# Optimization experiments

Hardware: AMD Instinct MI355X
Metric: run time of the kernel (lower is better)

Reference implementation:

```python
import jax, jax.numpy as jnp
import numpy as np

B, T, F, U = 64, 256, 64, 512  # batch, bid_sequence, features, lstm units


def setup_inputs() -> dict:
    key = jax.random.key(0)
    ks = jax.random.split(key, 8)
    sc = 0.05
    return {
        "inputs": jax.random.normal(ks[0], (B, T, F), jnp.float32),
        "kernel": jax.random.normal(ks[1], (F, 4 * U), jnp.float32) * sc,      # LSTM input kernel (i,f,c,o)
        "rec_kernel": jax.random.normal(ks[2], (U, 4 * U), jnp.float32) * sc,  # LSTM recurrent kernel
        "bias": jax.random.normal(ks[3], (4 * U,), jnp.float32) * sc,          # LSTM bias
        "att_W": jax.random.normal(ks[4], (T, T), jnp.float32) * sc,           # row t = weights of attention_denses[t] (first t cols used)
        "att_b": jax.random.normal(ks[5], (T,), jnp.float32) * sc,             # bias of attention_denses[t]
        "out_W": jax.random.normal(ks[6], (U,), jnp.float32) * sc,             # final Dense(1) kernel
        "out_b": jax.random.normal(ks[7], (), jnp.float32) * sc,               # final Dense(1) bias
    }


def reference(inputs, kernel, rec_kernel, bias, att_W, att_b, out_W, out_b):
    Bs, Ts, _ = inputs.shape
    Us = rec_kernel.shape[0]

    # ---- LSTM (keras LSTMCell, gate order i,f,c,o; sigmoid/tanh) ----
    xz = jnp.einsum('btf,fg->btg', inputs, kernel) + bias  # precompute input projection

    def step(carry, z):
        h, c = carry
        g = z + h @ rec_kernel
        i, f, gc, o = jnp.split(g, 4, axis=-1)
        c = jax.nn.sigmoid(f) * c + jax.nn.sigmoid(i) * jnp.tanh(gc)
        h = jax.nn.sigmoid(o) * jnp.tanh(c)
        return (h, c), h

    init = (jnp.zeros((Bs, Us), inputs.dtype), jnp.zeros((Bs, Us), inputs.dtype))
    _, hs = jax.lax.scan(step, init, jnp.swapaxes(xz, 0, 1))
    x = jnp.swapaxes(hs, 0, 1)  # (B, T, U)

    # ---- attention_loop ----
    # keras Attention([x[:t], [x[t]]]) softmaxes over a single key -> weights are
    # exactly 1, so attn output is x[t] tiled t times; transpose + Dense_t(1)
    # collapses to sum(att_W[t, :t]) * x[t] + att_b[t]. Step 0 passes x[0] through.
    t_idx = jnp.arange(Ts)
    tri = (t_idx[None, :] < t_idx[:, None]).astype(x.dtype)  # row t: first t cols valid
    coef = jnp.where(t_idx == 0, jnp.asarray(1.0, x.dtype), jnp.sum(att_W * tri, axis=1))
    shift = jnp.where(t_idx == 0, jnp.asarray(0.0, x.dtype), att_b)
    att = x * coef[None, :, None] + shift[None, :, None]  # (B, T, U)

    # ---- final Dense(1) + reshape + sigmoid ----
    return jax.nn.sigmoid(jnp.einsum('btu,u->bt', att, out_W) + out_b)  # (B, T)
```

## Files before the change

kernel.cpp:

```cpp
#include <hip/hip_runtime.h>
#include <hip/hip_bf16.h>
#include <string.h>

#define B_ 64
#define T_ 256
#define F_ 64
#define U_ 512
#define G4_ 2048
#define KTOT 576
#define KSTEPS 18

typedef __attribute__((ext_vector_type(8))) short short8;
typedef __attribute__((ext_vector_type(4))) float v4f;
typedef __attribute__((ext_vector_type(4))) int i4;
typedef unsigned short u16;

__device__ __forceinline__ float bf2f(u16 b) {
    unsigned int x = ((unsigned int)b) << 16;
    float f; memcpy(&f, &x, 4); return f;
}
__device__ __forceinline__ u16 f2bf(float f) {
    __hip_bfloat16 h = __float2bfloat16(f);
    u16 b; memcpy(&b, &h, 2); return b;
}
__device__ __forceinline__ float sigmoidf_(float x) { return 1.f / (1.f + __expf(-x)); }
__device__ __forceinline__ float tanhf_(float x) {
    float xc = fminf(15.f, fmaxf(-15.f, x));
    float e = __expf(2.f * xc);
    return (e - 1.f) / (e + 1.f);
}

__device__ __forceinline__ float ldany(const void* p, size_t i, int fg) {
    return fg ? ((const float*)p)[i] : bf2f(((const u16*)p)[i]);
}

#define WS_FLAG   0
#define WS_XB     64
#define WS_WP     2097216
#define WS_H2     4456512
#define WS_DOT    4718656
#define WS_BIASF  4784192
#define WS_ATTWF  4792384
#define WS_ATTBF  5054528
#define WS_OUTWF  5055552
#define WS_OUTBF  5057600
#define WS_NEED   5057920

__global__ __launch_bounds__(256) void detect(const unsigned int* __restrict__ w,
                                              int* __restrict__ flag) {
    __shared__ int votes;
    if (threadIdx.x == 0) votes = 0;
    __syncthreads();
    unsigned int v = w[threadIdx.x];
    int e = (v >> 7) & 0xFF;
    if (e >= 100 && e <= 135) atomicAdd(&votes, 1);
    __syncthreads();
    if (threadIdx.x == 0) *flag = (votes < 200) ? 1 : 0;
}

__global__ __launch_bounds__(256) void convert(const void* __restrict__ x,
                                               const void* __restrict__ bias,
                                               const void* __restrict__ attW,
                                               const void* __restrict__ attb,
                                               const void* __restrict__ outW,
                                               const void* __restrict__ outb,
                                               const int* __restrict__ flag,
                                               u16* __restrict__ xb,
                                               float* __restrict__ biasf,
                                               float* __restrict__ attWf,
                                               float* __restrict__ attbf,
                                               float* __restrict__ outWf,
                                               float* __restrict__ outbf,
                                               float* __restrict__ dot,
                                               unsigned int* __restrict__ h2z) {
    int fg = *flag;
    size_t i = (size_t)blockIdx.x * 256 + threadIdx.x;
    if (i < 1048576) {
        float v = ldany(x, i, fg);
        int b = (int)(i >> 14), t = (int)((i >> 6) & 255), f = (int)(i & 63);
        xb[((size_t)t * B_ + b) * F_ + f] = f2bf(v);
        return;
    }
    i -= 1048576;
    if (i < 2048)  { biasf[i] = ldany(bias, i, fg); return; }
    i -= 2048;
    if (i < 65536) { attWf[i] = ldany(attW, i, fg); return; }
    i -= 65536;
    if (i < 256)   { attbf[i] = ldany(attb, i, fg); return; }
    i -= 256;
    if (i < 512)   { outWf[i] = ldany(outW, i, fg); return; }
    i -= 512;
    if (i < 1)     { outbf[i] = ldany(outb, i, fg); return; }
    i -= 1;
    if (i < 16384) { dot[i] = 0.f; return; }
    i -= 16384;
    if (i < 32768) { h2z[i] = 0u; return; }
}

__global__ __launch_bounds__(256) void pack_w(const void* __restrict__ kin,
                                              const void* __restrict__ krec,
                                              const int* __restrict__ flag,
                                              u16* __restrict__ Wp) {
    int fg = *flag;
    int gid = blockIdx.x * 256 + threadIdx.x;
    int lane = gid & 63;
    int frag = gid >> 6;
    int nt = frag / KSTEPS;
    int ks = frag - nt * KSTEPS;
    int kbase = ks * 32 + (lane >> 4) * 8;
    int cp = nt * 16 + (lane & 15);
    int u = cp >> 2, gate = cp & 3;
    int C = gate * U_ + u;
    short8 v;
    for (int j = 0; j < 8; j++) {
        int k = kbase + j;
        float w = (k < F_) ? ldany(kin, (size_t)k * G4_ + C, fg)
                           : ldany(krec, (size_t)(k - F_) * G4_ + C, fg);
        v[j] = (short)f2bf(w);
    }
    *reinterpret_cast<short8*>(Wp + (size_t)gid * 8) = v;
}

__global__ __launch_bounds__(512, 2) void lstm_persist(const u16* __restrict__ xb,
                                                       const float* __restrict__ biasf,
                                                       const float* __restrict__ outWf,
                                                       const u16* __restrict__ Wp,
                                                       u16* __restrict__ h2,
                                                       float* __restrict__ dot) {
    __shared__ __align__(16) u16 stage[16 * 520];
    __shared__ __align__(16) float gbuf[16][164];
    __shared__ float dp[32][16];

    int tid = threadIdx.x;
    int bid = blockIdx.x;
    int rg = bid & 3;
    int gu = bid >> 2;
    int w = tid >> 6, l = tid & 63;
    int nt = gu * 8 + w;

    short8 W[KSTEPS];
    #pragma unroll
    for (int ks = 0; ks < KSTEPS; ks++)
        W[ks] = *reinterpret_cast<const short8*>(Wp + ((size_t)(nt * KSTEPS + ks) * 64 + l) * 8);

    int arow = rg * 16 + (l & 15);
    int koff = (l >> 4) * 8;
    int plr = 2 * w + (l >> 5);
    int pcol = (l & 31) * 16;
    int er = tid >> 5;
    int ui = tid & 31;
    int unit = gu * 32 + ui;
    float bia = biasf[0 * U_ + unit], bif = biasf[1 * U_ + unit];
    float big = biasf[2 * U_ + unit], bio = biasf[3 * U_ + unit];
    float wout = outWf[unit];
    float c = 0.f;

    for (int t = 0; t < T_; t++) {
        u16* hcur = h2 + (size_t)(t & 1) * (B_ * U_);
        const u16* hprev = h2 + (size_t)((t + 1) & 1) * (B_ * U_);
        unsigned int wtag = ((unsigned)(t >> 1) & 1u) ^ 1u;
        unsigned int rpat = ((((unsigned)(t - 1) >> 1) & 1u) ^ 1u) * 0x00010001u;

        i4 q0, q1;
        {
            const void* bp = (const void*)(hprev + (size_t)(rg * 16 + plr) * U_ + pcol);
            int spins = 0;
            for (;;) {
                asm volatile(
                    "global_load_dwordx4 %0, %2, off sc0 sc1\n\t"
                    "global_load_dwordx4 %1, %2, off offset:16 sc0 sc1\n\t"
                    "s_waitcnt vmcnt(0)"
                    : "=v"(q0), "=v"(q1) : "v"(bp) : "memory");
                if (t == 0) break;
                unsigned bad = 0;
                bad |= (((unsigned)q0[0]) ^ rpat) & 0x00010001u;
                bad |= (((unsigned)q0[1]) ^ rpat) & 0x00010001u;
                bad |= (((unsigned)q0[2]) ^ rpat) & 0x00010001u;
                bad |= (((unsigned)q0[3]) ^ rpat) & 0x00010001u;
                bad |= (((unsigned)q1[0]) ^ rpat) & 0x00010001u;
                bad |= (((unsigned)q1[1]) ^ rpat) & 0x00010001u;
                bad |= (((unsigned)q1[2]) ^ rpat) & 0x00010001u;
                bad |= (((unsigned)q1[3]) ^ rpat) & 0x00010001u;
                if (__ballot(bad == 0) == ~0ull) break;
                if (++spins > (1 << 14)) break;
                __builtin_amdgcn_s_sleep(2);
            }
        }
        *reinterpret_cast<i4*>(&stage[plr * 520 + pcol])     = q0;
        *reinterpret_cast<i4*>(&stage[plr * 520 + pcol + 8]) = q1;
        __syncthreads();

        const u16* xrow = xb + ((size_t)t * B_ + arow) * F_;
        short8 a0 = *reinterpret_cast<const short8*>(xrow + koff);
        short8 a1 = *reinterpret_cast<const short8*>(xrow + 32 + koff);
        v4f acc0 = {0.f, 0.f, 0.f, 0.f}, acc1 = {0.f, 0.f, 0.f, 0.f};
        acc0 = __builtin_amdgcn_mfma_f32_16x16x32_bf16(a0, W[0], acc0, 0, 0, 0);
        acc1 = __builtin_amdgcn_mfma_f32_16x16x32_bf16(a1, W[1], acc1, 0, 0, 0);
        #pragma unroll
        for (int ks = 2; ks < KSTEPS; ks += 2) {
            short8 ah0 = *reinterpret_cast<const short8*>(
                &stage[(l & 15) * 520 + (ks - 2) * 32 + koff]);
            short8 ah1 = *reinterpret_cast<const short8*>(
                &stage[(l & 15) * 520 + (ks - 1) * 32 + koff]);
            acc0 = __builtin_amdgcn_mfma_f32_16x16x32_bf16(ah0, W[ks],     acc0, 0, 0, 0);
            acc1 = __builtin_amdgcn_mfma_f32_16x16x32_bf16(ah1, W[ks + 1], acc1, 0, 0, 0);
        }
        v4f acc = acc0 + acc1;

        {
            int c0 = 16 * w + (l & 15);
            int coff = 5 * (c0 >> 2) + (c0 & 3);
            int rb = (l >> 4) * 4;
            #pragma unroll
            for (int rr = 0; rr < 4; rr++)
                gbuf[rb + rr][coff] = acc[rr];
        }
        __syncthreads();

        {
            const float* gr = &gbuf[er][5 * ui];
            float ig = sigmoidf_(gr[0] + bia);
            float fg = sigmoidf_(gr[1] + bif);
            float gc = tanhf_(gr[2] + big);
            float og = sigmoidf_(gr[3] + bio);
            c = fg * c + ig * gc;
            float h = og * tanhf_(c);

            float hp = __shfl_xor(h, 1, 64);
            if ((ui & 1) == 0) {
                unsigned int pk = (unsigned int)(((unsigned)f2bf(h)  & 0xFFFEu) | wtag)
                                | ((unsigned int)(((unsigned)f2bf(hp) & 0xFFFEu) | wtag) << 16);
                void* sp = (void*)(hcur + (size_t)(rg * 16 + er) * U_ + unit);
                asm volatile("global_store_dword %0, %1, off sc0 sc1"
                             :: "v"(sp), "v"(pk) : "memory");
            }

            float s = h * wout;
            s += __shfl_xor(s, 1, 64);
            s += __shfl_xor(s, 2, 64);
            s += __shfl_xor(s, 4, 64);
            s += __shfl_xor(s, 8, 64);
            s += __shfl_xor(s, 16, 64);
            if (ui == 0) dp[t & 31][er] = s;
        }

        if ((t & 31) == 31) {
            __syncthreads();
            int t0 = t - 31;
            int tt = tid >> 4, row = tid & 15;
            atomicAdd(&dot[(size_t)(rg * 16 + row) * T_ + (t0 + tt)], dp[tt][row]);
        }
    }
}

__global__ __launch_bounds__(256) void finale(const float* __restrict__ attWf,
                                              const float* __restrict__ attbf,
                                              const float* __restrict__ outWf,
                                              const float* __restrict__ outbf,
                                              const float* __restrict__ dot,
                                              const int* __restrict__ flag,
                                              void* __restrict__ out) {
    __shared__ float red[256];
    int t = blockIdx.x, tid = threadIdx.x;
    int fg = *flag;

    float v = (tid < t) ? attWf[(size_t)t * T_ + tid] : 0.f;
    red[tid] = v; __syncthreads();
    for (int s = 128; s > 0; s >>= 1) { if (tid < s) red[tid] += red[tid + s]; __syncthreads(); }
    float coef = (t == 0) ? 1.f : red[0];
    __syncthreads();
    red[tid] = outWf[tid] + outWf[tid + 256]; __syncthreads();
    for (int s = 128; s > 0; s >>= 1) { if (tid < s) red[tid] += red[tid + s]; __syncthreads(); }
    float sumW = red[0];

    float base = ((t == 0) ? 0.f : attbf[t]) * sumW + outbf[0];

    if (tid < B_) {
        float s = sigmoidf_(coef * dot[(size_t)tid * T_ + t] + base);
        size_t idx = (size_t)tid * T_ + t;
        if (fg) ((float*)out)[idx] = s;
        else    ((u16*)out)[idx] = f2bf(s);
    }
}

extern "C" void kernel_launch(void* const* d_in, const int* in_sizes, int n_in,
                              void* d_out, int out_size, void* d_ws, size_t ws_size,
                              hipStream_t stream) {
    const void* x    = d_in[0];
    const void* kin  = d_in[1];
    const void* krec = d_in[2];
    const void* bias = d_in[3];
    const void* attW = d_in[4];
    const void* attb = d_in[5];
    const void* outW = d_in[6];
    const void* outb = d_in[7];

    if (ws_size < (size_t)WS_NEED) return;

    char* ws = (char*)d_ws;
    int*   flag  = (int*)(ws + WS_FLAG);
    u16*   xb    = (u16*)(ws + WS_XB);
    u16*   Wp    = (u16*)(ws + WS_WP);
    u16*   h2    = (u16*)(ws + WS_H2);
    float* dot   = (float*)(ws + WS_DOT);
    float* biasf = (float*)(ws + WS_BIASF);
    float* attWf = (float*)(ws + WS_ATTWF);
    float* attbf = (float*)(ws + WS_ATTBF);
    float* outWf = (float*)(ws + WS_OUTWF);
    float* outbf = (float*)(ws + WS_OUTBF);

    detect<<<1, 256, 0, stream>>>((const unsigned int*)kin, flag);
    convert<<<4556, 256, 0, stream>>>(x, bias, attW, attb, outW, outb, flag,
                                      xb, biasf, attWf, attbf, outWf, outbf, dot,
                                      (unsigned int*)h2);
    pack_w<<<576, 256, 0, stream>>>(kin, krec, flag, Wp);
    lstm_persist<<<64, 512, 0, stream>>>(xb, biasf, outWf, Wp, h2, dot);
    finale<<<256, 256, 0, stream>>>(attWf, attbf, outWf, outbf, dot, flag, d_out);
}
```

Measured before the change: 686.3 us.

## Replace in-band parity tags with per-wave sequence counters for cross-block sync

The old scheme embedded a parity bit in each bf16 hidden value and spun re-loading the whole h tile until all tags matched. Now each wave publishes a step counter to a small seq array after its h stores drain, and readers poll 16 counters before doing a single load of h. This removes repeated polling of the full h tile and the precision loss from stealing the low mantissa bit. In exchange it adds a store-wait and a separate flag write per step, plus a dependency chain of flag then data, and it relies on correct memory ordering between the data and flag stores.

```diff
diff --git a/kernel.cpp b/kernel.cpp
--- a/kernel.cpp
+++ b/kernel.cpp
@@ -44,12 +44,16 @@
 #define WS_ATTBF  5054528
 #define WS_OUTWF  5055552
 #define WS_OUTBF  5057600
-#define WS_NEED   5057920
+#define WS_SEQ    5057920
+#define WS_NEED   5059968
 
 __global__ __launch_bounds__(256) void detect(const unsigned int* __restrict__ w,
-                                              int* __restrict__ flag) {
+                                              int* __restrict__ flag,
+                                              int* __restrict__ seq) {
     __shared__ int votes;
     if (threadIdx.x == 0) votes = 0;
+    seq[threadIdx.x] = 0;
+    seq[threadIdx.x + 256] = 0;
     __syncthreads();
     unsigned int v = w[threadIdx.x];
     int e = (v >> 7) & 0xFF;
@@ -126,7 +130,8 @@
                                                        const float* __restrict__ outWf,
                                                        const u16* __restrict__ Wp,
                                                        u16* __restrict__ h2,
-                                                       float* __restrict__ dot) {
+                                                       float* __restrict__ dot,
+                                                       int* __restrict__ seq) {
     __shared__ __align__(16) u16 stage[16 * 520];
     __shared__ __align__(16) float gbuf[16][164];
     __shared__ float dp[32][16];
@@ -155,36 +160,38 @@
     float wout = outWf[unit];
     float c = 0.f;
 
+    const int* sq_rd = seq + rg * 128 + w * 16;
+    int*       sq_wr = seq + rg * 128 + w * 16 + gu;
+
     for (int t = 0; t < T_; t++) {
         u16* hcur = h2 + (size_t)(t & 1) * (B_ * U_);
         const u16* hprev = h2 + (size_t)((t + 1) & 1) * (B_ * U_);
-        unsigned int wtag = ((unsigned)(t >> 1) & 1u) ^ 1u;
-        unsigned int rpat = ((((unsigned)(t - 1) >> 1) & 1u) ^ 1u) * 0x00010001u;
+
+        if (t > 0) {
+            int spins = 0;
+            bool mine = (l < 16);
+            const void* cp = (const void*)(sq_rd + (l & 15));
+            for (;;) {
+                int sv = t;
+                if (mine) {
+                    asm volatile("global_load_dword %0, %1, off sc0 sc1\n\t"
+                                 "s_waitcnt vmcnt(0)"
+                                 : "=v"(sv) : "v"(cp) : "memory");
+                }
+                if (__ballot(sv >= t) == ~0ull) break;
+                if (++spins > (1 << 14)) break;
+                __builtin_amdgcn_s_sleep(2);
+            }
+        }
 
         i4 q0, q1;
         {
             const void* bp = (const void*)(hprev + (size_t)(rg * 16 + plr) * U_ + pcol);
-            int spins = 0;
-            for (;;) {
-                asm volatile(
-                    "global_load_dwordx4 %0, %2, off sc0 sc1\n\t"
-                    "global_load_dwordx4 %1, %2, off offset:16 sc0 sc1\n\t"
-                    "s_waitcnt vmcnt(0)"
-                    : "=v"(q0), "=v"(q1) : "v"(bp) : "memory");
-                if (t == 0) break;
-                unsigned bad = 0;
-                bad |= (((unsigned)q0[0]) ^ rpat) & 0x00010001u;
-                bad |= (((unsigned)q0[1]) ^ rpat) & 0x00010001u;
-                bad |= (((unsigned)q0[2]) ^ rpat) & 0x00010001u;
-                bad |= (((unsigned)q0[3]) ^ rpat) & 0x00010001u;
-                bad |= (((unsigned)q1[0]) ^ rpat) & 0x00010001u;
-                bad |= (((unsigned)q1[1]) ^ rpat) & 0x00010001u;
-                bad |= (((unsigned)q1[2]) ^ rpat) & 0x00010001u;
-                bad |= (((unsigned)q1[3]) ^ rpat) & 0x00010001u;
-                if (__ballot(bad == 0) == ~0ull) break;
-                if (++spins > (1 << 14)) break;
-                __builtin_amdgcn_s_sleep(2);
-            }
+            asm volatile(
+                "global_load_dwordx4 %0, %2, off sc0 sc1\n\t"
+                "global_load_dwordx4 %1, %2, off offset:16 sc0 sc1\n\t"
+                "s_waitcnt vmcnt(0)"
+                : "=v"(q0), "=v"(q1) : "v"(bp) : "memory");
         }
         *reinterpret_cast<i4*>(&stage[plr * 520 + pcol])     = q0;
         *reinterpret_cast<i4*>(&stage[plr * 520 + pcol + 8]) = q1;
@@ -226,10 +233,10 @@
             c = fg * c + ig * gc;
             float h = og * tanhf_(c);
 
-            float hp = __shfl_xor(h, 1, 64);
+            float hpv = __shfl_xor(h, 1, 64);
             if ((ui & 1) == 0) {
-                unsigned int pk = (unsigned int)(((unsigned)f2bf(h)  & 0xFFFEu) | wtag)
-                                | ((unsigned int)(((unsigned)f2bf(hp) & 0xFFFEu) | wtag) << 16);
+                unsigned int pk = (unsigned int)f2bf(h)
+                                | ((unsigned int)f2bf(hpv) << 16);
                 void* sp = (void*)(hcur + (size_t)(rg * 16 + er) * U_ + unit);
                 asm volatile("global_store_dword %0, %1, off sc0 sc1"
                              :: "v"(sp), "v"(pk) : "memory");
@@ -242,6 +249,13 @@
             s += __shfl_xor(s, 8, 64);
             s += __shfl_xor(s, 16, 64);
             if (ui == 0) dp[t & 31][er] = s;
+        }
+
+        asm volatile("s_waitcnt vmcnt(0)" ::: "memory");
+        if (l == 0) {
+            int vv = t + 1;
+            asm volatile("global_store_dword %0, %1, off sc0 sc1"
+                         :: "v"((void*)sq_wr), "v"(vv) : "memory");
         }
 
         if ((t & 31) == 31) {
@@ -308,12 +322,13 @@
     float* attbf = (float*)(ws + WS_ATTBF);
     float* outWf = (float*)(ws + WS_OUTWF);
     float* outbf = (float*)(ws + WS_OUTBF);
-
-    detect<<<1, 256, 0, stream>>>((const unsigned int*)kin, flag);
+    int*   seq   = (int*)(ws + WS_SEQ);
+
+    detect<<<1, 256, 0, stream>>>((const unsigned int*)kin, flag, seq);
     convert<<<4556, 256, 0, stream>>>(x, bias, attW, attb, outW, outb, flag,
                                       xb, biasf, attWf, attbf, outWf, outbf, dot,
                                       (unsigned int*)h2);
     pack_w<<<576, 256, 0, stream>>>(kin, krec, flag, Wp);
-    lstm_persist<<<64, 512, 0, stream>>>(xb, biasf, outWf, Wp, h2, dot);
+    lstm_persist<<<64, 512, 0, stream>>>(xb, biasf, outWf, Wp, h2, dot, seq);
     finale<<<256, 256, 0, stream>>>(attWf, attbf, outWf, outbf, dot, flag, d_out);
 }
```

Result: slower. 966.2 us (+40.8%).

## Fuse preprocessing, weight packing and epilogue into single persistent LSTM kernel

Applied to the files above, without the earlier changes.

Replaces the detect, convert, pack_w, lstm_persist and finale kernels with one persistent kernel. Each block detects the dtype, packs its recurrent and input weight fragments straight from the raw inputs into registers, and loads and converts x per timestep. The x MFMAs are issued before waiting on the previous h. A done counter lets the gu==0 blocks run the attention/sigmoid epilogue after all blocks finish. This removes four kernel launches and the full round trip of x and W through workspace. In exchange it adds strided uncoalesced weight loads at kernel start, per-step fp32 x loads, and a spin-wait for the epilogue.

```diff
diff --git a/kernel.cpp b/kernel.cpp
--- a/kernel.cpp
+++ b/kernel.cpp
@@ -34,126 +34,89 @@
     return fg ? ((const float*)p)[i] : bf2f(((const u16*)p)[i]);
 }
 
-#define WS_FLAG   0
-#define WS_XB     64
-#define WS_WP     2097216
-#define WS_H2     4456512
-#define WS_DOT    4718656
-#define WS_BIASF  4784192
-#define WS_ATTWF  4792384
-#define WS_ATTBF  5054528
-#define WS_OUTWF  5055552
-#define WS_OUTBF  5057600
-#define WS_NEED   5057920
-
-__global__ __launch_bounds__(256) void detect(const unsigned int* __restrict__ w,
-                                              int* __restrict__ flag) {
-    __shared__ int votes;
-    if (threadIdx.x == 0) votes = 0;
-    __syncthreads();
-    unsigned int v = w[threadIdx.x];
-    int e = (v >> 7) & 0xFF;
-    if (e >= 100 && e <= 135) atomicAdd(&votes, 1);
-    __syncthreads();
-    if (threadIdx.x == 0) *flag = (votes < 200) ? 1 : 0;
-}
-
-__global__ __launch_bounds__(256) void convert(const void* __restrict__ x,
-                                               const void* __restrict__ bias,
-                                               const void* __restrict__ attW,
-                                               const void* __restrict__ attb,
-                                               const void* __restrict__ outW,
-                                               const void* __restrict__ outb,
-                                               const int* __restrict__ flag,
-                                               u16* __restrict__ xb,
-                                               float* __restrict__ biasf,
-                                               float* __restrict__ attWf,
-                                               float* __restrict__ attbf,
-                                               float* __restrict__ outWf,
-                                               float* __restrict__ outbf,
-                                               float* __restrict__ dot,
-                                               unsigned int* __restrict__ h2z) {
-    int fg = *flag;
-    size_t i = (size_t)blockIdx.x * 256 + threadIdx.x;
-    if (i < 1048576) {
-        float v = ldany(x, i, fg);
-        int b = (int)(i >> 14), t = (int)((i >> 6) & 255), f = (int)(i & 63);
-        xb[((size_t)t * B_ + b) * F_ + f] = f2bf(v);
-        return;
-    }
-    i -= 1048576;
-    if (i < 2048)  { biasf[i] = ldany(bias, i, fg); return; }
-    i -= 2048;
-    if (i < 65536) { attWf[i] = ldany(attW, i, fg); return; }
-    i -= 65536;
-    if (i < 256)   { attbf[i] = ldany(attb, i, fg); return; }
-    i -= 256;
-    if (i < 512)   { outWf[i] = ldany(outW, i, fg); return; }
-    i -= 512;
-    if (i < 1)     { outbf[i] = ldany(outb, i, fg); return; }
-    i -= 1;
-    if (i < 16384) { dot[i] = 0.f; return; }
-    i -= 16384;
-    if (i < 32768) { h2z[i] = 0u; return; }
-}
-
-__global__ __launch_bounds__(256) void pack_w(const void* __restrict__ kin,
-                                              const void* __restrict__ krec,
-                                              const int* __restrict__ flag,
-                                              u16* __restrict__ Wp) {
-    int fg = *flag;
-    int gid = blockIdx.x * 256 + threadIdx.x;
-    int lane = gid & 63;
-    int frag = gid >> 6;
-    int nt = frag / KSTEPS;
-    int ks = frag - nt * KSTEPS;
-    int kbase = ks * 32 + (lane >> 4) * 8;
-    int cp = nt * 16 + (lane & 15);
-    int u = cp >> 2, gate = cp & 3;
-    int C = gate * U_ + u;
-    short8 v;
-    for (int j = 0; j < 8; j++) {
-        int k = kbase + j;
-        float w = (k < F_) ? ldany(kin, (size_t)k * G4_ + C, fg)
-                           : ldany(krec, (size_t)(k - F_) * G4_ + C, fg);
-        v[j] = (short)f2bf(w);
-    }
-    *reinterpret_cast<short8*>(Wp + (size_t)gid * 8) = v;
-}
-
-__global__ __launch_bounds__(512, 2) void lstm_persist(const u16* __restrict__ xb,
-                                                       const float* __restrict__ biasf,
-                                                       const float* __restrict__ outWf,
-                                                       const u16* __restrict__ Wp,
-                                                       u16* __restrict__ h2,
-                                                       float* __restrict__ dot) {
+#define WS_DOT   0
+#define WS_H2    65536
+#define WS_DONE  196608
+#define WS_NEED  196672
+
+__global__ __launch_bounds__(512, 2) void lstm_fused(const void* __restrict__ x,
+                                                     const void* __restrict__ kin,
+                                                     const void* __restrict__ krec,
+                                                     const void* __restrict__ bias,
+                                                     const void* __restrict__ attW,
+                                                     const void* __restrict__ attb,
+                                                     const void* __restrict__ outW,
+                                                     const void* __restrict__ outb,
+                                                     u16* __restrict__ h2,
+                                                     float* __restrict__ dot,
+                                                     int* __restrict__ done,
+                                                     void* __restrict__ outp) {
     __shared__ __align__(16) u16 stage[16 * 520];
     __shared__ __align__(16) float gbuf[16][164];
     __shared__ float dp[32][16];
+    __shared__ int votes;
 
     int tid = threadIdx.x;
     int bid = blockIdx.x;
     int rg = bid & 3;
     int gu = bid >> 2;
     int w = tid >> 6, l = tid & 63;
+
+    if (tid == 0) votes = 0;
+    __syncthreads();
+    if (tid < 256) {
+        unsigned int v = ((const unsigned int*)kin)[tid];
+        int e = (v >> 7) & 0xFF;
+        if (e >= 100 && e <= 135) atomicAdd(&votes, 1);
+    }
+    __syncthreads();
+    const int fg = (votes < 200) ? 1 : 0;
+
     int nt = gu * 8 + w;
-
     short8 W[KSTEPS];
-    #pragma unroll
-    for (int ks = 0; ks < KSTEPS; ks++)
-        W[ks] = *reinterpret_cast<const short8*>(Wp + ((size_t)(nt * KSTEPS + ks) * 64 + l) * 8);
+    {
+        int cp = nt * 16 + (l & 15);
+        int u = cp >> 2, gate = cp & 3;
+        int C = gate * U_ + u;
+        int kb = (l >> 4) * 8;
+        #pragma unroll
+        for (int ks = 0; ks < KSTEPS; ks++) {
+            short8 v;
+            #pragma unroll
+            for (int j = 0; j < 8; j++) {
+                int k = ks * 32 + kb + j;
+                float wv = (k < F_) ? ldany(kin, (size_t)k * G4_ + C, fg)
+                                    : ldany(krec, (size_t)(k - F_) * G4_ + C, fg);
+                v[j] = (short)f2bf(wv);
+            }
+            W[ks] = v;
+        }
+    }
 
     int arow = rg * 16 + (l & 15);
     int koff = (l >> 4) * 8;
     int plr = 2 * w + (l >> 5);
     int pcol = (l & 31) * 16;
-    int er = tid >> 5;
-    int ui = tid & 31;
+    int er = tid >> 5, ui = tid & 31;
     int unit = gu * 32 + ui;
-    float bia = biasf[0 * U_ + unit], bif = biasf[1 * U_ + unit];
-    float big = biasf[2 * U_ + unit], bio = biasf[3 * U_ + unit];
-    float wout = outWf[unit];
+    float bia = ldany(bias, 0 * U_ + unit, fg), bif = ldany(bias, 1 * U_ + unit, fg);
+    float big = ldany(bias, 2 * U_ + unit, fg), bio = ldany(bias, 3 * U_ + unit, fg);
+    float wout = ldany(outW, unit, fg);
     float c = 0.f;
+
+    if (gu == 0) {
+        for (int i = tid; i < 16 * T_; i += 512) {
+            unsigned int z = 0;
+            void* zp = (void*)(dot + (size_t)(rg * 16 + (i >> 8)) * T_ + (i & 255));
+            asm volatile("global_store_dword %0, %1, off sc0 sc1" :: "v"(zp), "v"(z) : "memory");
+        }
+        if (tid == 0) {
+            unsigned int z = 0;
+            asm volatile("global_store_dword %0, %1, off sc0 sc1"
+                         :: "v"((void*)(done + rg)), "v"(z) : "memory");
+        }
+    }
+    asm volatile("s_waitcnt vmcnt(0)" ::: "memory");
 
     for (int t = 0; t < T_; t++) {
         u16* hcur = h2 + (size_t)(t & 1) * (B_ * U_);
@@ -161,8 +124,28 @@
         unsigned int wtag = ((unsigned)(t >> 1) & 1u) ^ 1u;
         unsigned int rpat = ((((unsigned)(t - 1) >> 1) & 1u) ^ 1u) * 0x00010001u;
 
-        i4 q0, q1;
+        short8 a0, a1;
         {
+            size_t xoff = ((size_t)arow * T_ + t) * F_;
+            if (fg) {
+                const float* xp = (const float*)x + xoff;
+                #pragma unroll
+                for (int j = 0; j < 8; j++) {
+                    a0[j] = (short)f2bf(xp[koff + j]);
+                    a1[j] = (short)f2bf(xp[32 + koff + j]);
+                }
+            } else {
+                const u16* xp = (const u16*)x + xoff;
+                a0 = *reinterpret_cast<const short8*>(xp + koff);
+                a1 = *reinterpret_cast<const short8*>(xp + 32 + koff);
+            }
+        }
+        v4f acc0 = {0.f, 0.f, 0.f, 0.f}, acc1 = {0.f, 0.f, 0.f, 0.f};
+        acc0 = __builtin_amdgcn_mfma_f32_16x16x32_bf16(a0, W[0], acc0, 0, 0, 0);
+        acc1 = __builtin_amdgcn_mfma_f32_16x16x32_bf16(a1, W[1], acc1, 0, 0, 0);
+
+        if (t > 0) {
+            i4 q0, q1;
             const void* bp = (const void*)(hprev + (size_t)(rg * 16 + plr) * U_ + pcol);
             int spins = 0;
             for (;;) {
@@ -171,7 +154,6 @@
                     "global_load_dwordx4 %1, %2, off offset:16 sc0 sc1\n\t"
                     "s_waitcnt vmcnt(0)"
                     : "=v"(q0), "=v"(q1) : "v"(bp) : "memory");
-                if (t == 0) break;
                 unsigned bad = 0;
                 bad |= (((unsigned)q0[0]) ^ rpat) & 0x00010001u;
                 bad |= (((unsigned)q0[1]) ^ rpat) & 0x00010001u;
@@ -185,25 +167,21 @@
                 if (++spins > (1 << 14)) break;
                 __builtin_amdgcn_s_sleep(2);
             }
-        }
-        *reinterpret_cast<i4*>(&stage[plr * 520 + pcol])     = q0;
-        *reinterpret_cast<i4*>(&stage[plr * 520 + pcol + 8]) = q1;
+            *reinterpret_cast<i4*>(&stage[plr * 520 + pcol])     = q0;
+            *reinterpret_cast<i4*>(&stage[plr * 520 + pcol + 8]) = q1;
+        }
         __syncthreads();
 
-        const u16* xrow = xb + ((size_t)t * B_ + arow) * F_;
-        short8 a0 = *reinterpret_cast<const short8*>(xrow + koff);
-        short8 a1 = *reinterpret_cast<const short8*>(xrow + 32 + koff);
-        v4f acc0 = {0.f, 0.f, 0.f, 0.f}, acc1 = {0.f, 0.f, 0.f, 0.f};
-        acc0 = __builtin_amdgcn_mfma_f32_16x16x32_bf16(a0, W[0], acc0, 0, 0, 0);
-        acc1 = __builtin_amdgcn_mfma_f32_16x16x32_bf16(a1, W[1], acc1, 0, 0, 0);
-        #pragma unroll
-        for (int ks = 2; ks < KSTEPS; ks += 2) {
-            short8 ah0 = *reinterpret_cast<const short8*>(
-                &stage[(l & 15) * 520 + (ks - 2) * 32 + koff]);
-            short8 ah1 = *reinterpret_cast<const short8*>(
-                &stage[(l & 15) * 520 + (ks - 1) * 32 + koff]);
-            acc0 = __builtin_amdgcn_mfma_f32_16x16x32_bf16(ah0, W[ks],     acc0, 0, 0, 0);
-            acc1 = __builtin_amdgcn_mfma_f32_16x16x32_bf16(ah1, W[ks + 1], acc1, 0, 0, 0);
+        if (t > 0) {
+            #pragma unroll
+            for (int ks = 2; ks < KSTEPS; ks += 2) {
+                short8 ah0 = *reinterpret_cast<const short8*>(
+                    &stage[(l & 15) * 520 + (ks - 2) * 32 + koff]);
+                short8 ah1 = *reinterpret_cast<const short8*>(
+                    &stage[(l & 15) * 520 + (ks - 1) * 32 + koff]);
+                acc0 = __builtin_amdgcn_mfma_f32_16x16x32_bf16(ah0, W[ks],     acc0, 0, 0, 0);
+                acc1 = __builtin_amdgcn_mfma_f32_16x16x32_bf16(ah1, W[ks + 1], acc1, 0, 0, 0);
+            }
         }
         v4f acc = acc0 + acc1;
 
@@ -220,16 +198,16 @@
         {
             const float* gr = &gbuf[er][5 * ui];
             float ig = sigmoidf_(gr[0] + bia);
-            float fg = sigmoidf_(gr[1] + bif);
+            float fgt = sigmoidf_(gr[1] + bif);
             float gc = tanhf_(gr[2] + big);
             float og = sigmoidf_(gr[3] + bio);
-            c = fg * c + ig * gc;
+            c = fgt * c + ig * gc;
             float h = og * tanhf_(c);
 
-            float hp = __shfl_xor(h, 1, 64);
+            float hpv = __shfl_xor(h, 1, 64);
             if ((ui & 1) == 0) {
-                unsigned int pk = (unsigned int)(((unsigned)f2bf(h)  & 0xFFFEu) | wtag)
-                                | ((unsigned int)(((unsigned)f2bf(hp) & 0xFFFEu) | wtag) << 16);
+                unsigned int pk = (unsigned int)(((unsigned)f2bf(h)   & 0xFFFEu) | wtag)
+                                | ((unsigned int)(((unsigned)f2bf(hpv) & 0xFFFEu) | wtag) << 16);
                 void* sp = (void*)(hcur + (size_t)(rg * 16 + er) * U_ + unit);
                 asm volatile("global_store_dword %0, %1, off sc0 sc1"
                              :: "v"(sp), "v"(pk) : "memory");
@@ -251,35 +229,62 @@
             atomicAdd(&dot[(size_t)(rg * 16 + row) * T_ + (t0 + tt)], dp[tt][row]);
         }
     }
-}
-
-__global__ __launch_bounds__(256) void finale(const float* __restrict__ attWf,
-                                              const float* __restrict__ attbf,
-                                              const float* __restrict__ outWf,
-                                              const float* __restrict__ outbf,
-                                              const float* __restrict__ dot,
-                                              const int* __restrict__ flag,
-                                              void* __restrict__ out) {
-    __shared__ float red[256];
-    int t = blockIdx.x, tid = threadIdx.x;
-    int fg = *flag;
-
-    float v = (tid < t) ? attWf[(size_t)t * T_ + tid] : 0.f;
-    red[tid] = v; __syncthreads();
-    for (int s = 128; s > 0; s >>= 1) { if (tid < s) red[tid] += red[tid + s]; __syncthreads(); }
-    float coef = (t == 0) ? 1.f : red[0];
+
+    asm volatile("s_waitcnt vmcnt(0)" ::: "memory");
     __syncthreads();
-    red[tid] = outWf[tid] + outWf[tid + 256]; __syncthreads();
-    for (int s = 128; s > 0; s >>= 1) { if (tid < s) red[tid] += red[tid + s]; __syncthreads(); }
-    float sumW = red[0];
-
-    float base = ((t == 0) ? 0.f : attbf[t]) * sumW + outbf[0];
-
-    if (tid < B_) {
-        float s = sigmoidf_(coef * dot[(size_t)tid * T_ + t] + base);
-        size_t idx = (size_t)tid * T_ + t;
-        if (fg) ((float*)out)[idx] = s;
-        else    ((u16*)out)[idx] = f2bf(s);
+    if (tid == 0) atomicAdd(done + rg, 1);
+    if (gu != 0) return;
+
+    if (tid == 0) {
+        int spins = 0;
+        const void* dq = (const void*)(done + rg);
+        for (;;) {
+            int dv;
+            asm volatile("global_load_dword %0, %1, off sc0 sc1\n\ts_waitcnt vmcnt(0)"
+                         : "=v"(dv) : "v"(dq) : "memory");
+            if (dv >= 16) break;
+            if (++spins > (1 << 16)) break;
+            __builtin_amdgcn_s_sleep(8);
+        }
+    }
+    __syncthreads();
+
+    if (tid < 256) {
+        int t = tid;
+        float s = 0.f;
+        for (int j = 0; j < t; j++) s += ldany(attW, (size_t)t * T_ + j, fg);
+        ((float*)stage)[t]       = (t == 0) ? 1.f : s;
+        ((float*)stage)[256 + t] = (t == 0) ? 0.f : ldany(attb, t, fg);
+    }
+    {
+        float* redf = &gbuf[0][0];
+        redf[tid] = ldany(outW, tid, fg);
+        __syncthreads();
+        for (int s = 256; s > 0; s >>= 1) {
+            if (tid < s) redf[tid] += redf[tid + s];
+            __syncthreads();
+        }
+        float sumW = redf[0];
+        float outb0 = ldany(outb, 0, fg);
+
+        int row = tid >> 5;
+        int t0 = (tid & 31) * 8;
+        i4 d0, d1;
+        const void* dpq = (const void*)(dot + (size_t)(rg * 16 + row) * T_ + t0);
+        asm volatile("global_load_dwordx4 %0, %2, off sc0 sc1\n\t"
+                     "global_load_dwordx4 %1, %2, off offset:16 sc0 sc1\n\t"
+                     "s_waitcnt vmcnt(0)"
+                     : "=v"(d0), "=v"(d1) : "v"(dpq) : "memory");
+        #pragma unroll
+        for (int j = 0; j < 8; j++) {
+            int t = t0 + j;
+            float d = (j < 4) ? ((float*)&d0)[j] : ((float*)&d1)[j - 4];
+            float sv = sigmoidf_(((float*)stage)[t] * d
+                                 + ((float*)stage)[256 + t] * sumW + outb0);
+            size_t idx = (size_t)(rg * 16 + row) * T_ + t;
+            if (fg) ((float*)outp)[idx] = sv;
+            else    ((u16*)outp)[idx] = f2bf(sv);
+        }
     }
 }
 
@@ -298,22 +303,10 @@
     if (ws_size < (size_t)WS_NEED) return;
 
     char* ws = (char*)d_ws;
-    int*   flag  = (int*)(ws + WS_FLAG);
-    u16*   xb    = (u16*)(ws + WS_XB);
-    u16*   Wp    = (u16*)(ws + WS_WP);
-    u16*   h2    = (u16*)(ws + WS_H2);
-    float* dot   = (float*)(ws + WS_DOT);
-    float* biasf = (float*)(ws + WS_BIASF);
-    float* attWf = (float*)(ws + WS_ATTWF);
-    float* attbf = (float*)(ws + WS_ATTBF);
-    float* outWf = (float*)(ws + WS_OUTWF);
-    float* outbf = (float*)(ws + WS_OUTBF);
-
-    detect<<<1, 256, 0, stream>>>((const unsigned int*)kin, flag);
-    convert<<<4556, 256, 0, stream>>>(x, bias, attW, attb, outW, outb, flag,
-                                      xb, biasf, attWf, attbf, outWf, outbf, dot,
-                                      (unsigned int*)h2);
-    pack_w<<<576, 256, 0, stream>>>(kin, krec, flag, Wp);
-    lstm_persist<<<64, 512, 0, stream>>>(xb, biasf, outWf, Wp, h2, dot);
-    finale<<<256, 256, 0, stream>>>(attWf, attbf, outWf, outbf, dot, flag, d_out);
-}
+    float* dot  = (float*)(ws + WS_DOT);
+    u16*   h2   = (u16*)(ws + WS_H2);
+    int*   done = (int*)(ws + WS_DONE);
+
+    lstm_fused<<<64, 512, 0, stream>>>(x, kin, krec, bias, attW, attb, outW, outb,
+                                       h2, dot, done, d_out);
+}
```

Result: slower. 769.7 us (+12.2%).
